# Kernel optimization log

Measured on AMD Instinct MI355X. Metric: run time of the kernel, lower is better.

## Reference

```python
import jax, jax.numpy as jnp
import numpy as np

B, N, ALPHA, K = 65536, 64, 4, 10  # batch, num_visible, alpha, gibbs steps
T = 1.0


def _circulant_fwd(kernel2d):
    # kernel2d: [alpha, N]. Mf[a, i, m] = kernel[a, (m - i) % N]
    # so that wv[b, a, i] = sum_j kernel[a, j] * v[b, (i + j) % N]  (torch conv1d on circularly padded v)
    i = jnp.arange(N)
    idx = (i[None, :] - i[:, None]) % N  # [i, m]
    return kernel2d[:, idx]


def _circulant_bwd(kernel2d):
    # Mb[a, i, m] = kernel[a, (i - 1 - m) % N]
    # matches torch: conv1d(circular_pad(h), flip(kernel)) -> wh[b, i] = sum_{a,j} kernel[a, N-1-j] * h[b, a, (i+j) % N]
    i = jnp.arange(N)
    idx = (i[:, None] - 1 - i[None, :]) % N  # [i, m]
    return kernel2d[:, idx]


def _free_energy(v, Mf, b_scalar, c_vec):
    # v: [B, N]; Mf: [alpha, N, N]; c_vec: [alpha]
    term1 = -b_scalar[0] * v.sum(axis=-1)                      # [B]
    wv = jnp.einsum('bm,aim->bai', v, Mf)                      # [B, alpha, N]
    term2 = -jax.nn.softplus(wv + c_vec[None, :, None]).sum(axis=(1, 2))
    return term1 + term2


def _gibbs(v0, Mf, Mb, b_scalar, c_vec, key):
    def step(carry, _):
        v, k = carry
        k, kh, kv = jax.random.split(k, 3)
        wv = jnp.einsum('bm,aim->bai', v, Mf)                  # [B, alpha, N]
        p_h = jax.nn.sigmoid((wv + c_vec[None, :, None]) / T)
        h = jax.random.bernoulli(kh, p_h).astype(v.dtype)      # [B, alpha, N]
        wh = jnp.einsum('bam,aim->bi', h, Mb)                  # [B, N]
        p_v = jax.nn.sigmoid((wh + b_scalar[0]) / T)
        v_next = jax.random.bernoulli(kv, p_v).astype(v.dtype)
        return (v_next, k), None
    (v, _), _ = jax.lax.scan(step, (v0, key), None, length=K)
    return v


def setup_inputs() -> dict:
    key = jax.random.key(0)
    k1, k2, k3, k4 = jax.random.split(key, 4)
    v_data = jax.random.randint(k1, (B, N), 0, 2).astype(jnp.float32)  # binary spins
    kernel = 0.05 * jax.random.normal(k2, (1, ALPHA, N), dtype=jnp.float32)
    # torch init is zeros for b/c; small random values used so the reference exercises non-trivial math
    b_scalar = 0.01 * jax.random.normal(k3, (1,), dtype=jnp.float32)
    c_vector = 0.01 * jax.random.normal(k4, (1, ALPHA), dtype=jnp.float32)
    return {"v_data": v_data, "kernel": kernel, "b_scalar": b_scalar, "c_vector": c_vector}


def reference(v_data, kernel, b_scalar, c_vector):
    k2d = kernel[0]                # [alpha, N]
    c_vec = c_vector[0]            # [alpha]
    Mf = _circulant_fwd(k2d)       # [alpha, N, N]
    Mb = _circulant_bwd(k2d)       # [alpha, N, N]
    samp_key = jax.random.key(42)  # stands in for the torch Generator in aux_vars
    v_model = _gibbs(v_data, Mf, Mb, b_scalar, c_vec, samp_key)
    v_model = jax.lax.stop_gradient(v_model)  # .detach() in torch
    fe_data = _free_energy(v_data, Mf, b_scalar, c_vec)
    fe_model = _free_energy(v_model, Mf, b_scalar, c_vec)
    return (fe_data - fe_model).mean()
```

## Files before the change

kernel.cpp:

```cpp
#include <hip/hip_runtime.h>


#define KSTEPS 10
#define HALF_H 8388608u
#define HALF_V 2097152u

__device__ __forceinline__ void tf20(unsigned int k0, unsigned int k1,
                                     unsigned int x0, unsigned int x1,
                                     unsigned int &o0, unsigned int &o1)
{
  unsigned int k2 = k0 ^ k1 ^ 0x1BD11BDAu;
  x0 += k0; x1 += k1;
#define TFR(rot) { x0 += x1; x1 = (x1 << (rot)) | (x1 >> (32 - (rot))); x1 ^= x0; }
  TFR(13) TFR(15) TFR(26) TFR(6)
  x0 += k1; x1 += k2 + 1u;
  TFR(17) TFR(29) TFR(16) TFR(24)
  x0 += k2; x1 += k0 + 2u;
  TFR(13) TFR(15) TFR(26) TFR(6)
  x0 += k0; x1 += k1 + 3u;
  TFR(17) TFR(29) TFR(16) TFR(24)
  x0 += k1; x1 += k2 + 4u;
  TFR(13) TFR(15) TFR(26) TFR(6)
  x0 += k2; x1 += k0 + 5u;
#undef TFR
  o0 = x0; o1 = x1;
}

__device__ __forceinline__ float u01(unsigned int bits) {
  return __uint_as_float((bits >> 9) | 0x3F800000u) - 1.0f;
}

__device__ __forceinline__ float softplusf(float x) {
  return fmaxf(x, 0.0f) + log1pf(expf(-fabsf(x)));
}

__global__ void init_ws_kernel(float* ws) { ws[0] = 0.0f; }

__global__ __launch_bounds__(256, 2)
void rbm_valu_kernel(const float* __restrict__ vdat,
                     const float* __restrict__ kf,
                     const float* __restrict__ bsp,
                     const float* __restrict__ cvp,
                     float* __restrict__ ws)
{
  __shared__ __align__(16) float kd2[8][129][4];
  __shared__ unsigned int sK[4][KSTEPS];

  const int tid = threadIdx.x;
  const int gthread = blockIdx.x * 256 + tid;
  const int pair = gthread >> 3;
  const int q = gthread & 7;
  const int i0 = 8 * q;

  if (tid == 0) {
    unsigned int c0 = 0u, c1 = 42u;
    for (int t = 0; t < KSTEPS; ++t) {
      unsigned int Aa, Ab, Ba, Bb, Ca, Cb;
      tf20(c0, c1, 0u, 3u, Aa, Ab);
      tf20(c0, c1, 1u, 4u, Ba, Bb);
      tf20(c0, c1, 2u, 5u, Ca, Cb);
      sK[0][t] = Ca; sK[1][t] = Ab;
      sK[2][t] = Bb; sK[3][t] = Cb;
      c0 = Aa; c1 = Ba;
    }
  }
  for (int idx = tid; idx < 8 * 129; idx += 256) {
    const int cc = idx / 129;
    const int z = idx % 129;
    const int zz = z & 63;
    kd2[cc][z][0] = kf[zz];
    kd2[cc][z][1] = kf[64 + zz];
    kd2[cc][z][2] = kf[128 + zz];
    kd2[cc][z][3] = kf[192 + zz];
  }
  __syncthreads();

  const float4* kr = (const float4*)&kd2[q][0][0];

  unsigned int vw[2][2];
  for (int r = 0; r < 2; ++r) {
    const float* vp = vdat + (size_t)(pair + r * 32768) * 64;
    unsigned int w0 = 0u, w1 = 0u;
#pragma unroll
    for (int j = 0; j < 32; j += 4) {
      float4 f = *(const float4*)(vp + j);
      w0 |= ((unsigned int)(f.x != 0.0f)) << (j + 0);
      w0 |= ((unsigned int)(f.y != 0.0f)) << (j + 1);
      w0 |= ((unsigned int)(f.z != 0.0f)) << (j + 2);
      w0 |= ((unsigned int)(f.w != 0.0f)) << (j + 3);
      float4 g = *(const float4*)(vp + 32 + j);
      w1 |= ((unsigned int)(g.x != 0.0f)) << (j + 0);
      w1 |= ((unsigned int)(g.y != 0.0f)) << (j + 1);
      w1 |= ((unsigned int)(g.z != 0.0f)) << (j + 2);
      w1 |= ((unsigned int)(g.w != 0.0f)) << (j + 3);
    }
    vw[r][0] = w0; vw[r][1] = w1;
  }

  const float bs = bsp[0];
  const float cv[4] = {cvp[0], cvp[1], cvp[2], cvp[3]};

  float fe = 0.0f;
  if (q == 0)
    fe -= bs * (float)(__popc(vw[0][0]) + __popc(vw[0][1]) +
                       __popc(vw[1][0]) + __popc(vw[1][1]));

  unsigned int hw[2][2][4];

  for (int step = 0; step <= KSTEPS; ++step) {
    const bool fe_pass   = (step == KSTEPS);
    const bool data_pass = (step == 0);
    const unsigned int kh0 = sK[0][fe_pass ? 0 : step];
    const unsigned int kh1 = sK[1][fe_pass ? 0 : step];

    float acc[2][4][8] = {};
#pragma unroll
    for (int w = 0; w < 2; ++w) {
      const unsigned int b0 = vw[0][w], b1 = vw[1][w];
      const int base = 32 * w - i0 + 64;
#pragma unroll 4
      for (int mm = 0; mm < 32; ++mm) {
        float f0 = (float)((b0 >> mm) & 1u);
        float f1 = (float)((b1 >> mm) & 1u);
        const float4* kp = kr + (base + mm);
#pragma unroll
        for (int ii = 0; ii < 8; ++ii) {
          const float4 kv = kp[-ii];
          acc[0][0][ii] += f0 * kv.x; acc[0][1][ii] += f0 * kv.y;
          acc[0][2][ii] += f0 * kv.z; acc[0][3][ii] += f0 * kv.w;
          acc[1][0][ii] += f1 * kv.x; acc[1][1][ii] += f1 * kv.y;
          acc[1][2][ii] += f1 * kv.z; acc[1][3][ii] += f1 * kv.w;
        }
      }
    }

    if (fe_pass || data_pass) {
#pragma unroll
      for (int ii = 0; ii < 8; ++ii) {
        float s = 0.0f;
#pragma unroll
        for (int a = 0; a < 4; ++a) {
          float x0 = acc[0][a][ii] + cv[a];
          float x1 = acc[1][a][ii] + cv[a];
          s += softplusf(x0) + softplusf(x1);
        }
        fe += fe_pass ? s : -s;
      }
    }
    if (fe_pass) break;

    unsigned int hmy[2][4] = {{0u,0u,0u,0u},{0u,0u,0u,0u}};
#pragma unroll
    for (int ii = 0; ii < 8; ++ii) {
      const unsigned int base = (unsigned int)pair * 256u + (unsigned int)(i0 + ii);
#pragma unroll
      for (int a = 0; a < 4; ++a) {
        float x0 = acc[0][a][ii] + cv[a];
        float x1 = acc[1][a][ii] + cv[a];
        unsigned int cnt = base + (unsigned int)a * 64u;
        unsigned int r0, r1; tf20(kh0, kh1, cnt, cnt + HALF_H, r0, r1);
        float u0 = u01(r0), u1 = u01(r1);
        float e0 = __expf(-x0), e1 = __expf(-x1);
        hmy[0][a] |= ((fmaf(u0, e0, u0) < 1.0f) ? 1u : 0u) << ii;
        hmy[1][a] |= ((fmaf(u1, e1, u1) < 1.0f) ? 1u : 0u) << ii;
      }
    }

#pragma unroll
    for (int r = 0; r < 2; ++r)
#pragma unroll
      for (int a = 0; a < 4; ++a) {
        unsigned int my = hmy[r][a];
        unsigned int p1 = (unsigned int)__shfl_xor((int)my, 1);
        unsigned int v16 = (q & 1) ? (p1 | (my << 8)) : (my | (p1 << 8));
        unsigned int p2 = (unsigned int)__shfl_xor((int)v16, 2);
        unsigned int v32 = (q & 2) ? (p2 | (v16 << 16)) : (v16 | (p2 << 16));
        unsigned int p3 = (unsigned int)__shfl_xor((int)v32, 4);
        hw[0][r][a] = (q & 4) ? p3 : v32;
        hw[1][r][a] = (q & 4) ? v32 : p3;
      }

    const unsigned int kv0 = sK[2][step], kv1 = sK[3][step];
    float wh[2][8] = {};
#pragma unroll
    for (int w = 0; w < 2; ++w) {
      const unsigned int tA0 = hw[w][0][0], tA1 = hw[w][0][1];
      const unsigned int tA2 = hw[w][0][2], tA3 = hw[w][0][3];
      const unsigned int tB0 = hw[w][1][0], tB1 = hw[w][1][1];
      const unsigned int tB2 = hw[w][1][2], tB3 = hw[w][1][3];
      const int base2 = i0 + 63 - 32 * w;
#pragma unroll 4
      for (int mm = 0; mm < 32; ++mm) {
        float fA0 = (float)((tA0 >> mm) & 1u), fA1 = (float)((tA1 >> mm) & 1u);
        float fA2 = (float)((tA2 >> mm) & 1u), fA3 = (float)((tA3 >> mm) & 1u);
        float fB0 = (float)((tB0 >> mm) & 1u), fB1 = (float)((tB1 >> mm) & 1u);
        float fB2 = (float)((tB2 >> mm) & 1u), fB3 = (float)((tB3 >> mm) & 1u);
        const float4* kp = kr + (base2 - mm);
#pragma unroll
        for (int ii = 0; ii < 8; ++ii) {
          const float4 kv = kp[ii];
          wh[0][ii] += fA0 * kv.x + fA1 * kv.y + fA2 * kv.z + fA3 * kv.w;
          wh[1][ii] += fB0 * kv.x + fB1 * kv.y + fB2 * kv.z + fB3 * kv.w;
        }
      }
    }

    unsigned int vmy[2] = {0u, 0u};
#pragma unroll
    for (int ii = 0; ii < 8; ++ii) {
      unsigned int cnt = (unsigned int)pair * 64u + (unsigned int)(i0 + ii);
      unsigned int r0, r1; tf20(kv0, kv1, cnt, cnt + HALF_V, r0, r1);
      float u0 = u01(r0), u1 = u01(r1);
      float e0 = __expf(-(wh[0][ii] + bs)), e1 = __expf(-(wh[1][ii] + bs));
      vmy[0] |= ((fmaf(u0, e0, u0) < 1.0f) ? 1u : 0u) << ii;
      vmy[1] |= ((fmaf(u1, e1, u1) < 1.0f) ? 1u : 0u) << ii;
    }

#pragma unroll
    for (int r = 0; r < 2; ++r) {
      unsigned int my = vmy[r];
      unsigned int p1 = (unsigned int)__shfl_xor((int)my, 1);
      unsigned int v16 = (q & 1) ? (p1 | (my << 8)) : (my | (p1 << 8));
      unsigned int p2 = (unsigned int)__shfl_xor((int)v16, 2);
      unsigned int v32 = (q & 2) ? (p2 | (v16 << 16)) : (v16 | (p2 << 16));
      unsigned int p3 = (unsigned int)__shfl_xor((int)v32, 4);
      vw[r][0] = (q & 4) ? p3 : v32;
      vw[r][1] = (q & 4) ? v32 : p3;
    }
  }

  if (q == 0)
    fe += bs * (float)(__popc(vw[0][0]) + __popc(vw[0][1]) +
                       __popc(vw[1][0]) + __popc(vw[1][1]));

  for (int off = 32; off > 0; off >>= 1) fe += __shfl_down(fe, off);
  if ((tid & 63) == 0) atomicAdd(ws, fe);
}

__global__ void fin_kernel(const float* __restrict__ ws, float* __restrict__ out) {
  out[0] = ws[0] * (1.0f / 65536.0f);
}

extern "C" void kernel_launch(void* const* d_in, const int* in_sizes, int n_in,
                              void* d_out, int out_size, void* d_ws, size_t ws_size,
                              hipStream_t stream)
{
  (void)in_sizes; (void)n_in; (void)out_size; (void)ws_size;
  const float* vdat = (const float*)d_in[0];
  const float* kf   = (const float*)d_in[1];
  const float* bsp  = (const float*)d_in[2];
  const float* cvp  = (const float*)d_in[3];
  float* out = (float*)d_out;
  float* ws  = (float*)d_ws;

  init_ws_kernel<<<dim3(1), dim3(1), 0, stream>>>(ws);
  rbm_valu_kernel<<<dim3(1024), dim3(256), 0, stream>>>(vdat, kf, bsp, cvp, ws);
  fin_kernel<<<dim3(1), dim3(1), 0, stream>>>(ws, out);
}
```

Baseline: 1.056 ms.

## Use sliding register windows for kernel taps in forward and backward convolutions

The forward pass is split into two blocks of four output positions, shrinking the accumulator array, and each block keeps a rotating 4-entry register window of kernel float4 values. Each tap is now loaded once and reused across neighbouring outputs instead of being reloaded for every output. The backward pass uses an 8-entry rotating window the same way. Hidden sampling now runs per block right after accumulation. This cuts LDS/global loads and register pressure, but the forward v-bit loop runs twice and the window indexing relies on full unrolling to stay in registers.

Measured after the change: 1.338 ms. 26.7% more time.

```diff
diff --git a/kernel.cpp b/kernel.cpp
--- a/kernel.cpp
+++ b/kernel.cpp
@@ -113,58 +113,72 @@
     const unsigned int kh0 = sK[0][fe_pass ? 0 : step];
     const unsigned int kh1 = sK[1][fe_pass ? 0 : step];
 
-    float acc[2][4][8] = {};
-#pragma unroll
-    for (int w = 0; w < 2; ++w) {
-      const unsigned int b0 = vw[0][w], b1 = vw[1][w];
-      const int base = 32 * w - i0 + 64;
-#pragma unroll 4
-      for (int mm = 0; mm < 32; ++mm) {
-        float f0 = (float)((b0 >> mm) & 1u);
-        float f1 = (float)((b1 >> mm) & 1u);
-        const float4* kp = kr + (base + mm);
-#pragma unroll
-        for (int ii = 0; ii < 8; ++ii) {
-          const float4 kv = kp[-ii];
-          acc[0][0][ii] += f0 * kv.x; acc[0][1][ii] += f0 * kv.y;
-          acc[0][2][ii] += f0 * kv.z; acc[0][3][ii] += f0 * kv.w;
-          acc[1][0][ii] += f1 * kv.x; acc[1][1][ii] += f1 * kv.y;
-          acc[1][2][ii] += f1 * kv.z; acc[1][3][ii] += f1 * kv.w;
-        }
-      }
-    }
-
-    if (fe_pass || data_pass) {
-#pragma unroll
-      for (int ii = 0; ii < 8; ++ii) {
-        float s = 0.0f;
-#pragma unroll
-        for (int a = 0; a < 4; ++a) {
-          float x0 = acc[0][a][ii] + cv[a];
-          float x1 = acc[1][a][ii] + cv[a];
-          s += softplusf(x0) + softplusf(x1);
-        }
-        fe += fe_pass ? s : -s;
+    unsigned int hmy[2][4] = {{0u,0u,0u,0u},{0u,0u,0u,0u}};
+
+#pragma unroll 1
+    for (int blk = 0; blk < 2; ++blk) {
+      float acc[2][4][4] = {};
+#pragma unroll
+      for (int w = 0; w < 2; ++w) {
+        const unsigned int b0 = vw[0][w], b1 = vw[1][w];
+        const int basek = 32 * w - i0 - 4 * blk + 64;
+        float4 win[4];
+        win[1] = kr[basek - 3];
+        win[2] = kr[basek - 2];
+        win[3] = kr[basek - 1];
+        for (int mmo = 0; mmo < 32; mmo += 4) {
+#pragma unroll
+          for (int u = 0; u < 4; ++u) {
+            const int mm = mmo + u;
+            win[u] = kr[basek + mm];
+            const float f0 = (float)((b0 >> mm) & 1u);
+            const float f1 = (float)((b1 >> mm) & 1u);
+#pragma unroll
+            for (int ir = 0; ir < 4; ++ir) {
+              const float4 kv = win[(u - ir) & 3];
+              acc[0][0][ir] += f0 * kv.x; acc[0][1][ir] += f0 * kv.y;
+              acc[0][2][ir] += f0 * kv.z; acc[0][3][ir] += f0 * kv.w;
+              acc[1][0][ir] += f1 * kv.x; acc[1][1][ir] += f1 * kv.y;
+              acc[1][2][ir] += f1 * kv.z; acc[1][3][ir] += f1 * kv.w;
+            }
+          }
+        }
+      }
+
+      if (fe_pass || data_pass) {
+#pragma unroll
+        for (int ir = 0; ir < 4; ++ir) {
+          float s = 0.0f;
+#pragma unroll
+          for (int a = 0; a < 4; ++a) {
+            float x0 = acc[0][a][ir] + cv[a];
+            float x1 = acc[1][a][ir] + cv[a];
+            s += softplusf(x0) + softplusf(x1);
+          }
+          fe += fe_pass ? s : -s;
+        }
+      }
+      if (!fe_pass) {
+#pragma unroll
+        for (int ir = 0; ir < 4; ++ir) {
+          const int iia = 4 * blk + ir;
+          const unsigned int base = (unsigned int)pair * 256u +
+                                    (unsigned int)(i0 + iia);
+#pragma unroll
+          for (int a = 0; a < 4; ++a) {
+            float x0 = acc[0][a][ir] + cv[a];
+            float x1 = acc[1][a][ir] + cv[a];
+            unsigned int cnt = base + (unsigned int)a * 64u;
+            unsigned int r0, r1; tf20(kh0, kh1, cnt, cnt + HALF_H, r0, r1);
+            float u0 = u01(r0), u1 = u01(r1);
+            float e0 = __expf(-x0), e1 = __expf(-x1);
+            hmy[0][a] |= ((fmaf(u0, e0, u0) < 1.0f) ? 1u : 0u) << iia;
+            hmy[1][a] |= ((fmaf(u1, e1, u1) < 1.0f) ? 1u : 0u) << iia;
+          }
+        }
       }
     }
     if (fe_pass) break;
-
-    unsigned int hmy[2][4] = {{0u,0u,0u,0u},{0u,0u,0u,0u}};
-#pragma unroll
-    for (int ii = 0; ii < 8; ++ii) {
-      const unsigned int base = (unsigned int)pair * 256u + (unsigned int)(i0 + ii);
-#pragma unroll
-      for (int a = 0; a < 4; ++a) {
-        float x0 = acc[0][a][ii] + cv[a];
-        float x1 = acc[1][a][ii] + cv[a];
-        unsigned int cnt = base + (unsigned int)a * 64u;
-        unsigned int r0, r1; tf20(kh0, kh1, cnt, cnt + HALF_H, r0, r1);
-        float u0 = u01(r0), u1 = u01(r1);
-        float e0 = __expf(-x0), e1 = __expf(-x1);
-        hmy[0][a] |= ((fmaf(u0, e0, u0) < 1.0f) ? 1u : 0u) << ii;
-        hmy[1][a] |= ((fmaf(u1, e1, u1) < 1.0f) ? 1u : 0u) << ii;
-      }
-    }
 
 #pragma unroll
     for (int r = 0; r < 2; ++r)
@@ -188,19 +202,37 @@
       const unsigned int tA2 = hw[w][0][2], tA3 = hw[w][0][3];
       const unsigned int tB0 = hw[w][1][0], tB1 = hw[w][1][1];
       const unsigned int tB2 = hw[w][1][2], tB3 = hw[w][1][3];
-      const int base2 = i0 + 63 - 32 * w;
-#pragma unroll 4
-      for (int mm = 0; mm < 32; ++mm) {
-        float fA0 = (float)((tA0 >> mm) & 1u), fA1 = (float)((tA1 >> mm) & 1u);
-        float fA2 = (float)((tA2 >> mm) & 1u), fA3 = (float)((tA3 >> mm) & 1u);
-        float fB0 = (float)((tB0 >> mm) & 1u), fB1 = (float)((tB1 >> mm) & 1u);
-        float fB2 = (float)((tB2 >> mm) & 1u), fB3 = (float)((tB3 >> mm) & 1u);
-        const float4* kp = kr + (base2 - mm);
-#pragma unroll
-        for (int ii = 0; ii < 8; ++ii) {
-          const float4 kv = kp[ii];
-          wh[0][ii] += fA0 * kv.x + fA1 * kv.y + fA2 * kv.z + fA3 * kv.w;
-          wh[1][ii] += fB0 * kv.x + fB1 * kv.y + fB2 * kv.z + fB3 * kv.w;
+      const int b2 = i0 + 63 - 32 * w;
+      float4 win[8];
+      win[7] = kr[b2 + 1];
+      win[6] = kr[b2 + 2];
+      win[5] = kr[b2 + 3];
+      win[4] = kr[b2 + 4];
+      win[3] = kr[b2 + 5];
+      win[2] = kr[b2 + 6];
+      win[1] = kr[b2 + 7];
+      for (int mmo = 0; mmo < 32; mmo += 8) {
+#pragma unroll
+        for (int u = 0; u < 8; ++u) {
+          const int mm = mmo + u;
+          win[u] = kr[b2 - mm];
+          const float fA0 = (float)((tA0 >> mm) & 1u);
+          const float fA1 = (float)((tA1 >> mm) & 1u);
+          const float fA2 = (float)((tA2 >> mm) & 1u);
+          const float fA3 = (float)((tA3 >> mm) & 1u);
+          const float fB0 = (float)((tB0 >> mm) & 1u);
+          const float fB1 = (float)((tB1 >> mm) & 1u);
+          const float fB2 = (float)((tB2 >> mm) & 1u);
+          const float fB3 = (float)((tB3 >> mm) & 1u);
+#pragma unroll
+          for (int ir = 0; ir < 4; ++ir) {
+            const float4 kvA = win[(u - ir) & 7];
+            wh[0][ir] += fA0 * kvA.x + fA1 * kvA.y + fA2 * kvA.z + fA3 * kvA.w;
+            wh[1][ir] += fB0 * kvA.x + fB1 * kvA.y + fB2 * kvA.z + fB3 * kvA.w;
+            const float4 kvB = win[(u - ir - 4) & 7];
+            wh[0][ir + 4] += fA0 * kvB.x + fA1 * kvB.y + fA2 * kvB.z + fA3 * kvB.w;
+            wh[1][ir + 4] += fB0 * kvB.x + fB1 * kvB.y + fB2 * kvB.z + fB3 * kvB.w;
+          }
         }
       }
     }
```
